# Kernel optimization log

Hardware: AMD Instinct MI355X
Metric: run time of the kernel (lower is better)

The kernel has to match this reference:

```python
import jax, jax.numpy as jnp
import numpy as np

P_DIMS = [100, 100, 80, 60, 60]
P = sum(P_DIMS)  # 400
N_STREAMS = len(P_DIMS)
MEM_ITERS = 5
DECAY = 0.8
LR = 0.5        # hebbian_learning_rate
FORGET = 0.9999 # hebbian_forget_rate
NEG_SLOPE = 0.01


def _build_masks():
    idx = np.cumsum([0] + P_DIMS)
    hier = np.zeros((P, P), np.float32)
    for i in range(N_STREAMS):
        for j in range(i, N_STREAMS):
            hier[idx[i]:idx[i + 1], idx[j]:idx[j + 1]] = 1.0
    iters = [MEM_ITERS - f for f in range(N_STREAMS)]  # [5,4,3,2,1]
    rmasks = np.zeros((MEM_ITERS, P), np.float32)
    for it in range(MEM_ITERS):
        for s, r in enumerate(iters):
            if it < r:
                rmasks[it, idx[s]:idx[s + 1]] = 1.0
    return jnp.asarray(hier), jnp.asarray(rmasks)


def setup_inputs() -> dict:
    key = jax.random.key(0)
    k1, k2, k3, k4 = jax.random.split(key, 4)
    B = 512
    return {
        'M_prev': jax.random.normal(k1, (B, P, P), dtype=jnp.float32) * 0.1,
        'p_inferred': jax.random.normal(k2, (B, P), dtype=jnp.float32),
        'p_generated': jax.random.normal(k3, (B, P), dtype=jnp.float32),
        'query': jax.random.normal(k4, (B, P), dtype=jnp.float32),
    }


def reference(M_prev, p_inferred, p_generated, query):
    hier_mask, retrieval_masks = _build_masks()

    # Hebbian update: M = clamp(forget*M_prev + lr*(p-phat)(p+phat)^T, -1, 1) * hier_mask
    outer = (p_inferred - p_generated)[:, :, None] * (p_inferred + p_generated)[:, None, :]
    M = jnp.clip(FORGET * M_prev + LR * outer, -1.0, 1.0) * hier_mask

    # Hierarchical attractor retrieval
    h = jax.nn.leaky_relu(jnp.clip(query, -1.0, 1.0), NEG_SLOPE)

    def step(h, mask):
        mv = jnp.einsum('bpq,bq->bp', M, h)
        upd = jax.nn.leaky_relu(jnp.clip(DECAY * h + mv, -1.0, 1.0), NEG_SLOPE)
        return (1.0 - mask) * h + mask * upd, None

    h, _ = jax.lax.scan(step, h, retrieval_masks)
    return h
```

## Files before the change

kernel.cpp:

```cpp
#include <hip/hip_runtime.h>


#define PDIM 400
#define FORGET 0.9999f
#define LRATE  0.5f
#define DECAY  0.8f
#define SLOPE  0.01f

__device__ __forceinline__ float leaky_clip(float x) {
    x = fminf(fmaxf(x, -1.0f), 1.0f);
    return x > 0.0f ? x : SLOPE * x;
}

__device__ __forceinline__ float clamp1(float x) {
    return fminf(fmaxf(x, -1.0f), 1.0f);
}

__global__ __launch_bounds__(512, 4)
void hier_mem_kernel(const float* __restrict__ M_prev,
                     const float* __restrict__ p_inf,
                     const float* __restrict__ p_gen,
                     const float* __restrict__ query,
                     float* __restrict__ out)
{
    __shared__ float s_h[2][PDIM];
    __shared__ float s_b[PDIM];
    __shared__ float s_la[PDIM];

    const int b   = blockIdx.x;
    const int tid = threadIdx.x;
    const float* __restrict__ Mb = M_prev + (size_t)b * PDIM * PDIM;

    if (tid < PDIM) {
        const float pi = p_inf[b * PDIM + tid];
        const float pg = p_gen[b * PDIM + tid];
        s_la[tid]   = LRATE * (pi - pg);
        s_b[tid]    = pi + pg;
        s_h[0][tid] = leaky_clip(query[b * PDIM + tid]);
    }
    __syncthreads();

    const int group  = tid >> 4;
    const int lane16 = tid & 15;

    const int Rt[5] = {400, 340, 280, 200, 100};

    int cur = 0;
    #pragma unroll
    for (int t = 0; t < 5; ++t) {
        const int R = Rt[t];
        const float* __restrict__ h_old = s_h[cur];
        float* __restrict__ h_new = s_h[cur ^ 1];

        for (int p = group; p < R; p += 32) {
            const int cbeg = (p < 100) ? 0 : (p < 200) ? 100 :
                             (p < 280) ? 200 : (p < 340) ? 280 : 340;
            const int nf4 = (PDIM - cbeg) >> 2;
            const float la = s_la[p];

            const float4* __restrict__ rowp = (const float4*)(Mb + (size_t)p * PDIM + cbeg);
            const float4* __restrict__ hb4  = (const float4*)(h_old + cbeg);
            const float4* __restrict__ bb4  = (const float4*)(s_b + cbeg);

            float acc = 0.0f;
            for (int j = lane16; j < nf4; j += 16) {
                const float4 mp = rowp[j];
                const float4 hv = hb4[j];
                const float4 bv = bb4[j];
                const float m0 = clamp1(fmaf(FORGET, mp.x, la * bv.x));
                const float m1 = clamp1(fmaf(FORGET, mp.y, la * bv.y));
                const float m2 = clamp1(fmaf(FORGET, mp.z, la * bv.z));
                const float m3 = clamp1(fmaf(FORGET, mp.w, la * bv.w));
                acc = fmaf(m0, hv.x, acc);
                acc = fmaf(m1, hv.y, acc);
                acc = fmaf(m2, hv.z, acc);
                acc = fmaf(m3, hv.w, acc);
            }
            acc += __shfl_xor(acc, 1, 64);
            acc += __shfl_xor(acc, 2, 64);
            acc += __shfl_xor(acc, 4, 64);
            acc += __shfl_xor(acc, 8, 64);

            if (lane16 == 0) {
                h_new[p] = leaky_clip(fmaf(DECAY, h_old[p], acc));
            }
        }

        if (tid >= R && tid < PDIM) {
            h_new[tid] = h_old[tid];
        }
        __syncthreads();
        cur ^= 1;
    }

    if (tid < PDIM) {
        out[b * PDIM + tid] = s_h[cur][tid];
    }
}

extern "C" void kernel_launch(void* const* d_in, const int* in_sizes, int n_in,
                              void* d_out, int out_size, void* d_ws, size_t ws_size,
                              hipStream_t stream) {
    const float* M_prev = (const float*)d_in[0];
    const float* p_inf  = (const float*)d_in[1];
    const float* p_gen  = (const float*)d_in[2];
    const float* query  = (const float*)d_in[3];
    float* out = (float*)d_out;

    const int B = in_sizes[1] / PDIM;
    hipLaunchKernelGGL(hier_mem_kernel, dim3(B), dim3(512), 0, stream,
                       M_prev, p_inf, p_gen, query, out);
}
```

Measured before the change: 495.1 us.

## Use one wavefront per row with register-cached h and b and prefetch

Measured after the change: 494.2 us. About the same (-0.2%).

```diff
diff --git a/kernel.cpp b/kernel.cpp
--- a/kernel.cpp
+++ b/kernel.cpp
@@ -11,9 +11,22 @@
     x = fminf(fmaxf(x, -1.0f), 1.0f);
     return x > 0.0f ? x : SLOPE * x;
 }
-
 __device__ __forceinline__ float clamp1(float x) {
     return fminf(fmaxf(x, -1.0f), 1.0f);
+}
+
+__device__ __forceinline__ int c4beg(int p) {
+    return (p < 100) ? 0 : (p < 200) ? 25 : (p < 280) ? 50 : (p < 340) ? 70 : 85;
+}
+
+__device__ __forceinline__ float wave_sum(float x) {
+    x += __int_as_float(__builtin_amdgcn_update_dpp(0, __float_as_int(x), 0xB1,  0xf, 0xf, true));
+    x += __int_as_float(__builtin_amdgcn_update_dpp(0, __float_as_int(x), 0x4E,  0xf, 0xf, true));
+    x += __int_as_float(__builtin_amdgcn_update_dpp(0, __float_as_int(x), 0x141, 0xf, 0xf, true));
+    x += __int_as_float(__builtin_amdgcn_update_dpp(0, __float_as_int(x), 0x140, 0xf, 0xf, true));
+    x += __int_as_float(__builtin_amdgcn_update_dpp(0, __float_as_int(x), 0x142, 0xf, 0xf, true));
+    x += __int_as_float(__builtin_amdgcn_update_dpp(0, __float_as_int(x), 0x143, 0xf, 0xf, true));
+    return __int_as_float(__builtin_amdgcn_readlane(__float_as_int(x), 63));
 }
 
 __global__ __launch_bounds__(512, 4)
@@ -24,71 +37,94 @@
                      float* __restrict__ out)
 {
     __shared__ float s_h[2][PDIM];
-    __shared__ float s_b[PDIM];
     __shared__ float s_la[PDIM];
 
     const int b   = blockIdx.x;
     const int tid = threadIdx.x;
+    const int l   = tid & 63;
+    const int wid = tid >> 6;
     const float* __restrict__ Mb = M_prev + (size_t)b * PDIM * PDIM;
 
     if (tid < PDIM) {
         const float pi = p_inf[b * PDIM + tid];
         const float pg = p_gen[b * PDIM + tid];
         s_la[tid]   = LRATE * (pi - pg);
-        s_b[tid]    = pi + pg;
         s_h[0][tid] = leaky_clip(query[b * PDIM + tid]);
+    }
+
+    const float4 z4 = make_float4(0.f, 0.f, 0.f, 0.f);
+    const float4* __restrict__ pi4 = (const float4*)(p_inf + (size_t)b * PDIM);
+    const float4* __restrict__ pg4 = (const float4*)(p_gen + (size_t)b * PDIM);
+    float4 bA, bB = z4;
+    {
+        const float4 x = pi4[l], y = pg4[l];
+        bA = make_float4(x.x + y.x, x.y + y.y, x.z + y.z, x.w + y.w);
+        if (l < 36) {
+            const float4 u = pi4[64 + l], v = pg4[64 + l];
+            bB = make_float4(u.x + v.x, u.y + v.y, u.z + v.z, u.w + v.w);
+        }
     }
     __syncthreads();
 
-    const int group  = tid >> 4;
-    const int lane16 = tid & 15;
+    const int Rt[5] = {400, 340, 280, 200, 100};
+    int cur = 0;
 
-    const int Rt[5] = {400, 340, 280, 200, 100};
-
-    int cur = 0;
     #pragma unroll
     for (int t = 0; t < 5; ++t) {
         const int R = Rt[t];
-        const float* __restrict__ h_old = s_h[cur];
-        float* __restrict__ h_new = s_h[cur ^ 1];
+        const float* __restrict__ hcur = s_h[cur];
+        float* __restrict__ hnew = s_h[cur ^ 1];
 
-        for (int p = group; p < R; p += 32) {
-            const int cbeg = (p < 100) ? 0 : (p < 200) ? 100 :
-                             (p < 280) ? 200 : (p < 340) ? 280 : 340;
-            const int nf4 = (PDIM - cbeg) >> 2;
+        float4 hA = *(const float4*)(hcur + 4 * l);
+        float4 hB = z4;
+        if (l < 36) hB = *(const float4*)(hcur + 256 + 4 * l);
+
+        int p = wid;
+        int c4 = 0;
+        float4 cA = z4, cB = z4;
+        if (p < R) {
+            c4 = c4beg(p);
+            const float* __restrict__ row = Mb + (size_t)p * PDIM;
+            if (l >= c4)               cA = *(const float4*)(row + 4 * l);
+            if (l < 36 && 64 + l >= c4) cB = *(const float4*)(row + 256 + 4 * l);
+        }
+        while (p < R) {
+            const int pn = p + 8;
+            int c4n = 0;
+            float4 nA = z4, nB = z4;
+            if (pn < R) {
+                c4n = c4beg(pn);
+                const float* __restrict__ rn = Mb + (size_t)pn * PDIM;
+                if (l >= c4n)                nA = *(const float4*)(rn + 4 * l);
+                if (l < 36 && 64 + l >= c4n) nB = *(const float4*)(rn + 256 + 4 * l);
+            }
+
             const float la = s_la[p];
+            float acc = 0.f;
+            if (l >= c4) {
+                float m0 = clamp1(fmaf(FORGET, cA.x, la * bA.x));
+                float m1 = clamp1(fmaf(FORGET, cA.y, la * bA.y));
+                float m2 = clamp1(fmaf(FORGET, cA.z, la * bA.z));
+                float m3 = clamp1(fmaf(FORGET, cA.w, la * bA.w));
+                acc = fmaf(m0, hA.x, fmaf(m1, hA.y, fmaf(m2, hA.z, m3 * hA.w)));
+            }
+            if (l < 36 && 64 + l >= c4) {
+                float m0 = clamp1(fmaf(FORGET, cB.x, la * bB.x));
+                float m1 = clamp1(fmaf(FORGET, cB.y, la * bB.y));
+                float m2 = clamp1(fmaf(FORGET, cB.z, la * bB.z));
+                float m3 = clamp1(fmaf(FORGET, cB.w, la * bB.w));
+                acc = fmaf(m0, hB.x, fmaf(m1, hB.y, fmaf(m2, hB.z, fmaf(m3, hB.w, acc))));
+            }
 
-            const float4* __restrict__ rowp = (const float4*)(Mb + (size_t)p * PDIM + cbeg);
-            const float4* __restrict__ hb4  = (const float4*)(h_old + cbeg);
-            const float4* __restrict__ bb4  = (const float4*)(s_b + cbeg);
+            const float tot = wave_sum(acc);
+            if (l == 0) {
+                hnew[p] = leaky_clip(fmaf(DECAY, hcur[p], tot));
+            }
 
-            float acc = 0.0f;
-            for (int j = lane16; j < nf4; j += 16) {
-                const float4 mp = rowp[j];
-                const float4 hv = hb4[j];
-                const float4 bv = bb4[j];
-                const float m0 = clamp1(fmaf(FORGET, mp.x, la * bv.x));
-                const float m1 = clamp1(fmaf(FORGET, mp.y, la * bv.y));
-                const float m2 = clamp1(fmaf(FORGET, mp.z, la * bv.z));
-                const float m3 = clamp1(fmaf(FORGET, mp.w, la * bv.w));
-                acc = fmaf(m0, hv.x, acc);
-                acc = fmaf(m1, hv.y, acc);
-                acc = fmaf(m2, hv.z, acc);
-                acc = fmaf(m3, hv.w, acc);
-            }
-            acc += __shfl_xor(acc, 1, 64);
-            acc += __shfl_xor(acc, 2, 64);
-            acc += __shfl_xor(acc, 4, 64);
-            acc += __shfl_xor(acc, 8, 64);
-
-            if (lane16 == 0) {
-                h_new[p] = leaky_clip(fmaf(DECAY, h_old[p], acc));
-            }
+            p = pn; c4 = c4n; cA = nA; cB = nB;
         }
 
-        if (tid >= R && tid < PDIM) {
-            h_new[tid] = h_old[tid];
-        }
+        if (tid >= R && tid < PDIM) hnew[tid] = hcur[tid];
         __syncthreads();
         cur ^= 1;
     }
```
